# Kernel optimization log

Hardware: AMD Instinct MI355X
Metric: run time of the kernel (lower is better)

## Reference

```python
import jax, jax.numpy as jnp
import numpy as np

KEY_DIM = 512
VALUE_DIM = 128
CAPACITY = 500000
N_RETRIEVE = 16
LN_EPS = 1e-5
NORM_EPS = 1e-12


def _l2norm(x, axis=-1):
    # F.normalize: x / max(||x||, eps)
    n = jnp.sqrt(jnp.sum(x * x, axis=axis, keepdims=True))
    return x / jnp.maximum(n, NORM_EPS)


def setup_inputs() -> dict:
    key = jax.random.key(0)
    ks = jax.random.split(key, 5)
    s = 1.0 / np.sqrt(KEY_DIM)
    return {
        "query": jax.random.normal(ks[0], (1, KEY_DIM), jnp.float32),
        "W1": jax.random.normal(ks[1], (KEY_DIM, KEY_DIM), jnp.float32) * s,
        "b1": jnp.zeros((KEY_DIM,), jnp.float32),
        "W2": jax.random.normal(ks[2], (KEY_DIM, KEY_DIM), jnp.float32) * s,
        "b2": jnp.zeros((KEY_DIM,), jnp.float32),
        "gamma": jnp.ones((KEY_DIM,), jnp.float32),
        "beta": jnp.zeros((KEY_DIM,), jnp.float32),
        "keys": jax.random.normal(ks[3], (CAPACITY, KEY_DIM), jnp.float32),
        "values": jax.random.normal(ks[4], (CAPACITY, VALUE_DIM), jnp.float32),
    }


def reference(query, W1, b1, W2, b2, gamma, beta, keys, values):
    # read path detaches the query before projecting
    q = jax.lax.stop_gradient(query)                      # [1, D]
    h = jax.nn.silu(q @ W1.T + b1) @ W2.T + b2            # key_proj
    mu = jnp.mean(h, axis=-1, keepdims=True)
    var = jnp.var(h, axis=-1, keepdims=True)              # biased, like torch LN
    ln = (h - mu) / jnp.sqrt(var + LN_EPS) * gamma + beta
    qn = _l2norm(ln)[0]                                   # [D]
    kn = _l2norm(keys, axis=-1)                           # [N, D]
    sim = kn @ qn                                         # [N] cosine similarity
    top_sim, top_idx = jax.lax.top_k(sim, N_RETRIEVE)     # [k]
    attn = jax.nn.softmax(top_sim, axis=0)                # [k]
    vals = values[top_idx]                                # [k, V] gather
    out = attn @ vals                                     # [V] weighted sum
    return out
```

## Files before the change

kernel.cpp:

```cpp
#include <hip/hip_runtime.h>
#include <hip/hip_bf16.h>
#include <float.h>
#include <math.h>

#define KEY_DIM   512
#define VALUE_DIM 128
#define CAPACITY  500000
#define NRET      16

#define SUBROWS   8
#define NBLKS     512
#define NSUB      (CAPACITY / SUBROWS)
#define RING      4

#define AS3 __attribute__((address_space(3)))
#define AS1 __attribute__((address_space(1)))

__device__ __forceinline__ float wave_sum(float x) {
#pragma unroll
    for (int s = 32; s > 0; s >>= 1) x += __shfl_xor(x, s);
    return x;
}

template <bool SILU>
__global__ __launch_bounds__(256) void matvec512(
        const float* __restrict__ W, const float* __restrict__ x,
        const float* __restrict__ b, float* __restrict__ y) {
    const int wid  = threadIdx.x >> 6;
    const int lane = threadIdx.x & 63;
    const int r = blockIdx.x * 4 + wid;

    const float4* Wr = (const float4*)(W + (size_t)r * KEY_DIM);
    const float4* xv = (const float4*)x;

    float4 w0 = Wr[lane], w1 = Wr[lane + 64];
    float4 x0 = xv[lane], x1 = xv[lane + 64];

    float dot = w0.x * x0.x + w0.y * x0.y + w0.z * x0.z + w0.w * x0.w
              + w1.x * x1.x + w1.y * x1.y + w1.z * x1.z + w1.w * x1.w;
    dot = wave_sum(dot);

    if (lane == 0) {
        float v = dot + b[r];
        if (SILU) v = v / (1.0f + expf(-v));
        y[r] = v;
    }
}

__global__ __launch_bounds__(512) void ln_l2norm(
        const float* __restrict__ h, const float* __restrict__ gamma,
        const float* __restrict__ beta, float* __restrict__ qn) {
    __shared__ float s1[8], s2[8];
    const int t = threadIdx.x;
    const int wid = t >> 6, lane = t & 63;

    float x = h[t];
    float a = x, bb = x * x;
#pragma unroll
    for (int s = 32; s > 0; s >>= 1) { a += __shfl_xor(a, s); bb += __shfl_xor(bb, s); }
    if (lane == 0) { s1[wid] = a; s2[wid] = bb; }
    __syncthreads();

    float suma = 0.f, sumb = 0.f;
#pragma unroll
    for (int i = 0; i < 8; ++i) { suma += s1[i]; sumb += s2[i]; }
    float mu  = suma * (1.0f / KEY_DIM);
    float var = sumb * (1.0f / KEY_DIM) - mu * mu;
    float ln  = (x - mu) / sqrtf(var + 1e-5f) * gamma[t] + beta[t];

    float c = wave_sum(ln * ln);
    __syncthreads();
    if (lane == 0) s1[wid] = c;
    __syncthreads();
    float ss = 0.f;
#pragma unroll
    for (int i = 0; i < 8; ++i) ss += s1[i];
    float n = fmaxf(sqrtf(ss), 1e-12f);
    qn[t] = ln / n;
}

__global__ __launch_bounds__(256) void sim_topk(
        const float* __restrict__ keys, const float* __restrict__ qn,
        float* __restrict__ cand_v, int* __restrict__ cand_i) {
    __shared__ float kl[RING][SUBROWS][KEY_DIM];
    __shared__ float bv[64];
    __shared__ int   bi[64];

    const int tid  = threadIdx.x;
    const int w    = tid >> 6;
    const int lane = tid & 63;
    const int m    = lane & 31;
    const int rsel = lane >> 5;
    const int bid  = blockIdx.x;
    const int ns   = (NSUB - bid + NBLKS - 1) / NBLKS;
    const int s0   = (int)(((unsigned)bid * 7919u) % (unsigned)ns);

    float4 qr[4];
    {
        const float4* q4 = (const float4*)qn;
#pragma unroll
        for (int j = 0; j < 4; ++j) qr[j] = q4[4 * m + j];
    }

    int srcoff0, srcoff1;
    {
        int p0 = lane,      g0 = p0 >> 2, sl0 = p0 & 3;
        int p1 = 64 + lane, g1 = p1 >> 2, sl1 = p1 & 3;
        srcoff0 = (4 * g0 + ((sl0 - (g0 >> 1)) & 3)) * 16;
        srcoff1 = (4 * g1 + ((sl1 - (g1 >> 1)) & 3)) * 16;
    }
    int roff[4];
#pragma unroll
    for (int j = 0; j < 4; ++j) roff[j] = (4 * m + ((j + (m >> 1)) & 3)) * 16;

    float v[16]; int id[16];
#pragma unroll
    for (int j = 0; j < 16; ++j) { v[j] = -FLT_MAX; id[j] = 0x7fffffff; }

    auto stage = [&](int G, int slot) {
#pragma unroll
        for (int i = 0; i < 4; ++i) {
            const int rl = 2 * w + (i >> 1);
            const int h  = i & 1;
            const char* gp = (const char*)(keys + ((size_t)G * SUBROWS + rl) * KEY_DIM)
                             + (h ? srcoff1 : srcoff0);
            float* lp = &kl[slot][rl][h * 256];
            __builtin_amdgcn_global_load_lds((const AS1 float*)gp, (AS3 float*)lp,
                                             16, 0, 0);
        }
    };

    auto compute = [&](int G, int slot) {
        const char* rowbase = (const char*)&kl[slot][2 * w + rsel][0];
        float dot = 0.f, ss = 0.f;
#pragma unroll
        for (int j = 0; j < 4; ++j) {
            float4 k = *(const float4*)(rowbase + roff[j]);
            float4 q = qr[j];
            dot += k.x * q.x + k.y * q.y + k.z * q.z + k.w * q.w;
            ss  += k.x * k.x + k.y * k.y + k.z * k.z + k.w * k.w;
        }
#pragma unroll
        for (int s = 16; s > 0; s >>= 1) {
            dot += __shfl_xor(dot, s);
            ss  += __shfl_xor(ss, s);
        }
        float sim = dot / fmaxf(sqrtf(ss), 1e-12f);
#pragma unroll
        for (int q = 0; q < 2; ++q) {
            float sq = __shfl(sim, q * 32);
            if (sq > v[15]) {
                float cv = sq; int ci = G * SUBROWS + 2 * w + q;
#pragma unroll
                for (int jj = 0; jj < 16; ++jj) {
                    if (cv > v[jj]) {
                        float tv = v[jj]; int ti = id[jj];
                        v[jj] = cv; id[jj] = ci; cv = tv; ci = ti;
                    }
                }
            }
        }
    };

    {
        int se = s0;
        stage(bid + se * NBLKS, 0);
        se = (se + 1 >= ns) ? 0 : se + 1;
        stage(bid + se * NBLKS, 1);
        se = (se + 1 >= ns) ? 0 : se + 1;
        stage(bid + se * NBLKS, 2);
    }

    int scur = s0;
    int spre = s0 + 3; if (spre >= ns) spre -= ns;

#pragma unroll 1
    for (int s = 0; s < ns; ++s) {
        stage(bid + spre * NBLKS, (s + 3) & 3);
        spre = (spre + 1 >= ns) ? 0 : spre + 1;
        asm volatile("s_waitcnt vmcnt(12)" ::: "memory");
        __builtin_amdgcn_sched_barrier(0);
        compute(bid + scur * NBLKS, s & 3);
        __builtin_amdgcn_sched_barrier(0);
        scur = (scur + 1 >= ns) ? 0 : scur + 1;
    }

    asm volatile("s_waitcnt vmcnt(0)" ::: "memory");

    if (lane == 0) {
#pragma unroll
        for (int j = 0; j < 16; ++j) { bv[w * 16 + j] = v[j]; bi[w * 16 + j] = id[j]; }
    }
    __syncthreads();
    if (w == 0) {
        float lv = bv[lane]; int li = bi[lane];
        for (int rr = 0; rr < NRET; ++rr) {
            float mv = lv; int mi = li;
#pragma unroll
            for (int s = 32; s > 0; s >>= 1) {
                float ov = __shfl_xor(mv, s); int oi = __shfl_xor(mi, s);
                if (ov > mv || (ov == mv && oi < mi)) { mv = ov; mi = oi; }
            }
            if (lane == 0) {
                cand_v[bid * NRET + rr] = mv;
                cand_i[bid * NRET + rr] = mi;
            }
            if (lv == mv && li == mi) { lv = -FLT_MAX; li = 0x7fffffff; }
        }
    }
}

__global__ __launch_bounds__(256) void merge_out(
        const float* __restrict__ cand_v, const int* __restrict__ cand_i,
        const float* __restrict__ values, float* __restrict__ out) {
    const int tid  = threadIdx.x;
    const int wid  = tid >> 6;
    const int lane = tid & 63;
    const int M4 = (NBLKS * NRET) / 4;

    float v[16]; int id[16];
#pragma unroll
    for (int j = 0; j < 16; ++j) { v[j] = -FLT_MAX; id[j] = 0x7fffffff; }

    const float4* cv4 = (const float4*)cand_v;
    const int4*   ci4 = (const int4*)cand_i;
    for (int c = tid; c < M4; c += 256) {
        float4 cv = cv4[c]; int4 ci = ci4[c];
        float cvs[4] = {cv.x, cv.y, cv.z, cv.w};
        int   cis[4] = {ci.x, ci.y, ci.z, ci.w};
#pragma unroll
        for (int u = 0; u < 4; ++u) {
            float cu = cvs[u]; int iu = cis[u];
            if (cu > v[15]) {
#pragma unroll
                for (int j = 0; j < 16; ++j) {
                    if (cu > v[j]) {
                        float tv = v[j]; int ti = id[j];
                        v[j] = cu; id[j] = iu; cu = tv; iu = ti;
                    }
                }
            }
        }
    }

    __shared__ float sv[64];
    __shared__ int   si[64];
    for (int rr = 0; rr < NRET; ++rr) {
        float mv = v[0]; int mi = id[0];
#pragma unroll
        for (int s = 32; s > 0; s >>= 1) {
            float ov = __shfl_xor(mv, s); int oi = __shfl_xor(mi, s);
            if (ov > mv || (ov == mv && oi < mi)) { mv = ov; mi = oi; }
        }
        if (v[0] == mv && id[0] == mi) {
#pragma unroll
            for (int j = 0; j < 15; ++j) { v[j] = v[j + 1]; id[j] = id[j + 1]; }
            v[15] = -FLT_MAX; id[15] = 0x7fffffff;
        }
        if (lane == 0) { sv[wid * 16 + rr] = mv; si[wid * 16 + rr] = mi; }
    }
    __syncthreads();

    if (wid == 0) {
        float lv = sv[lane]; int li = si[lane];
        float sel_v = -FLT_MAX; int sel_i = 0;
        for (int rr = 0; rr < NRET; ++rr) {
            float mv = lv; int mi = li;
#pragma unroll
            for (int s = 32; s > 0; s >>= 1) {
                float ov = __shfl_xor(mv, s); int oi = __shfl_xor(mi, s);
                if (ov > mv || (ov == mv && oi < mi)) { mv = ov; mi = oi; }
            }
            if (lv == mv && li == mi) { lv = -FLT_MAX; li = 0x7fffffff; }
            if (lane == rr) { sel_v = mv; sel_i = mi; }
        }

        float m0 = __shfl(sel_v, 0);
        float e = (lane < NRET) ? expf(sel_v - m0) : 0.0f;
        float denom = wave_sum(e);

        float acc0 = 0.f, acc1 = 0.f;
        for (int rr = 0; rr < NRET; ++rr) {
            float ar = __shfl(e, rr) / denom;
            int   ir = __shfl(sel_i, rr);
            const float* vr = values + (size_t)ir * VALUE_DIM;
            acc0 += ar * vr[lane];
            acc1 += ar * vr[lane + 64];
        }
        out[lane]      = acc0;
        out[lane + 64] = acc1;
    }
}

extern "C" void kernel_launch(void* const* d_in, const int* in_sizes, int n_in,
                              void* d_out, int out_size, void* d_ws, size_t ws_size,
                              hipStream_t stream) {
    const float* query  = (const float*)d_in[0];
    const float* W1     = (const float*)d_in[1];
    const float* b1     = (const float*)d_in[2];
    const float* W2     = (const float*)d_in[3];
    const float* b2     = (const float*)d_in[4];
    const float* gamma  = (const float*)d_in[5];
    const float* beta   = (const float*)d_in[6];
    const float* keys   = (const float*)d_in[7];
    const float* values = (const float*)d_in[8];
    float* out = (float*)d_out;

    float* ws = (float*)d_ws;
    float* h1     = ws;
    float* h2     = ws + 512;
    float* qn     = ws + 1024;
    float* cand_v = ws + 2048;
    int*   cand_i = (int*)(ws + 2048 + NBLKS * NRET);

    matvec512<true ><<<128, 256, 0, stream>>>(W1, query, b1, h1);
    matvec512<false><<<128, 256, 0, stream>>>(W2, h1, b2, h2);
    ln_l2norm<<<1, 512, 0, stream>>>(h2, gamma, beta, qn);
    sim_topk<<<NBLKS, 256, 0, stream>>>(keys, qn, cand_v, cand_i);
    merge_out<<<1, 256, 0, stream>>>(cand_v, cand_i, values, out);
}
```

Baseline: 262.5 us.

## Split similarity scan between LDS-staged blocks and direct-load register blocks

The similarity/top-k kernel now launches 768 blocks. Two thirds of them stream a fixed 70 sub-tiles of 8 rows each through a 3-slot LDS ring using global_load_lds. The remaining third read the tail rows straight into registers, four rows per wave, and reduce with wave shuffles. The intent is to run two load paths side by side and raise the memory-level parallelism of a bandwidth-bound 1 GB scan. The cost is a hard-coded row split, a smaller prefetch ring, and more candidates for the single-block merge.

```diff
diff --git a/kernel.cpp b/kernel.cpp
--- a/kernel.cpp
+++ b/kernel.cpp
@@ -8,10 +8,15 @@
 #define CAPACITY  500000
 #define NRET      16
 
-#define SUBROWS   8
-#define NBLKS     512
-#define NSUB      (CAPACITY / SUBROWS)
-#define RING      4
+#define NBLKD     512
+#define NBLKV     256
+#define NBLKT     (NBLKD + NBLKV)
+#define NSD       70
+#define NDROWS    (NBLKD * NSD * 8)
+#define ROFF      NDROWS
+#define NVROWS    (CAPACITY - NDROWS)
+#define VSWEEP    (NBLKV * 4 * 4)
+#define RING      3
 
 #define AS3 __attribute__((address_space(3)))
 #define AS1 __attribute__((address_space(1)))
@@ -79,113 +84,156 @@
     qn[t] = ln / n;
 }
 
-__global__ __launch_bounds__(256) void sim_topk(
+__global__ __launch_bounds__(256) void sim_hybrid(
         const float* __restrict__ keys, const float* __restrict__ qn,
         float* __restrict__ cand_v, int* __restrict__ cand_i) {
-    __shared__ float kl[RING][SUBROWS][KEY_DIM];
+    __shared__ float kl[RING][8][KEY_DIM];
     __shared__ float bv[64];
     __shared__ int   bi[64];
 
     const int tid  = threadIdx.x;
     const int w    = tid >> 6;
     const int lane = tid & 63;
-    const int m    = lane & 31;
-    const int rsel = lane >> 5;
     const int bid  = blockIdx.x;
-    const int ns   = (NSUB - bid + NBLKS - 1) / NBLKS;
-    const int s0   = (int)(((unsigned)bid * 7919u) % (unsigned)ns);
-
-    float4 qr[4];
-    {
-        const float4* q4 = (const float4*)qn;
-#pragma unroll
-        for (int j = 0; j < 4; ++j) qr[j] = q4[4 * m + j];
-    }
-
-    int srcoff0, srcoff1;
-    {
-        int p0 = lane,      g0 = p0 >> 2, sl0 = p0 & 3;
-        int p1 = 64 + lane, g1 = p1 >> 2, sl1 = p1 & 3;
-        srcoff0 = (4 * g0 + ((sl0 - (g0 >> 1)) & 3)) * 16;
-        srcoff1 = (4 * g1 + ((sl1 - (g1 >> 1)) & 3)) * 16;
-    }
-    int roff[4];
-#pragma unroll
-    for (int j = 0; j < 4; ++j) roff[j] = (4 * m + ((j + (m >> 1)) & 3)) * 16;
+    const int r3   = bid % 3;
 
     float v[16]; int id[16];
 #pragma unroll
     for (int j = 0; j < 16; ++j) { v[j] = -FLT_MAX; id[j] = 0x7fffffff; }
 
-    auto stage = [&](int G, int slot) {
-#pragma unroll
-        for (int i = 0; i < 4; ++i) {
-            const int rl = 2 * w + (i >> 1);
-            const int h  = i & 1;
-            const char* gp = (const char*)(keys + ((size_t)G * SUBROWS + rl) * KEY_DIM)
-                             + (h ? srcoff1 : srcoff0);
-            float* lp = &kl[slot][rl][h * 256];
-            __builtin_amdgcn_global_load_lds((const AS1 float*)gp, (AS3 float*)lp,
-                                             16, 0, 0);
-        }
-    };
-
-    auto compute = [&](int G, int slot) {
-        const char* rowbase = (const char*)&kl[slot][2 * w + rsel][0];
-        float dot = 0.f, ss = 0.f;
-#pragma unroll
-        for (int j = 0; j < 4; ++j) {
-            float4 k = *(const float4*)(rowbase + roff[j]);
-            float4 q = qr[j];
-            dot += k.x * q.x + k.y * q.y + k.z * q.z + k.w * q.w;
-            ss  += k.x * k.x + k.y * k.y + k.z * k.z + k.w * k.w;
-        }
-#pragma unroll
-        for (int s = 16; s > 0; s >>= 1) {
-            dot += __shfl_xor(dot, s);
-            ss  += __shfl_xor(ss, s);
-        }
-        float sim = dot / fmaxf(sqrtf(ss), 1e-12f);
-#pragma unroll
-        for (int q = 0; q < 2; ++q) {
-            float sq = __shfl(sim, q * 32);
-            if (sq > v[15]) {
-                float cv = sq; int ci = G * SUBROWS + 2 * w + q;
-#pragma unroll
-                for (int jj = 0; jj < 16; ++jj) {
-                    if (cv > v[jj]) {
-                        float tv = v[jj]; int ti = id[jj];
-                        v[jj] = cv; id[jj] = ci; cv = tv; ci = ti;
+    if (r3 < 2) {
+        const int d    = (bid / 3) * 2 + r3;
+        const int m    = lane & 31;
+        const int rsel = lane >> 5;
+        const int s0   = (d * 7919) % NSD;
+
+        float4 qr[4];
+        {
+            const float4* q4 = (const float4*)qn;
+#pragma unroll
+            for (int j = 0; j < 4; ++j) qr[j] = q4[4 * m + j];
+        }
+        int srcoff0, srcoff1;
+        {
+            int p0 = lane,      g0 = p0 >> 2, sl0 = p0 & 3;
+            int p1 = 64 + lane, g1 = p1 >> 2, sl1 = p1 & 3;
+            srcoff0 = (4 * g0 + ((sl0 - (g0 >> 1)) & 3)) * 16;
+            srcoff1 = (4 * g1 + ((sl1 - (g1 >> 1)) & 3)) * 16;
+        }
+        int roff[4];
+#pragma unroll
+        for (int j = 0; j < 4; ++j) roff[j] = (4 * m + ((j + (m >> 1)) & 3)) * 16;
+
+        auto stage = [&](int G, int slot) {
+#pragma unroll
+            for (int i = 0; i < 4; ++i) {
+                const int rl = 2 * w + (i >> 1);
+                const int h  = i & 1;
+                const char* gp = (const char*)(keys + ((size_t)G * 8 + rl) * KEY_DIM)
+                                 + (h ? srcoff1 : srcoff0);
+                float* lp = &kl[slot][rl][h * 256];
+                __builtin_amdgcn_global_load_lds((const AS1 float*)gp, (AS3 float*)lp,
+                                                 16, 0, 0);
+            }
+        };
+        auto compute = [&](int G, int slot) {
+            const char* rowbase = (const char*)&kl[slot][2 * w + rsel][0];
+            float dot = 0.f, ss = 0.f;
+#pragma unroll
+            for (int j = 0; j < 4; ++j) {
+                float4 k = *(const float4*)(rowbase + roff[j]);
+                float4 q = qr[j];
+                dot += k.x * q.x + k.y * q.y + k.z * q.z + k.w * q.w;
+                ss  += k.x * k.x + k.y * k.y + k.z * k.z + k.w * k.w;
+            }
+#pragma unroll
+            for (int s = 16; s > 0; s >>= 1) {
+                dot += __shfl_xor(dot, s);
+                ss  += __shfl_xor(ss, s);
+            }
+            float sim = dot / fmaxf(sqrtf(ss), 1e-12f);
+#pragma unroll
+            for (int q = 0; q < 2; ++q) {
+                float sq = __shfl(sim, q * 32);
+                if (sq > v[15]) {
+                    float cv = sq; int ci = G * 8 + 2 * w + q;
+#pragma unroll
+                    for (int jj = 0; jj < 16; ++jj) {
+                        if (cv > v[jj]) {
+                            float tv = v[jj]; int ti = id[jj];
+                            v[jj] = cv; id[jj] = ci; cv = tv; ci = ti;
+                        }
                     }
                 }
             }
-        }
-    };
-
-    {
-        int se = s0;
-        stage(bid + se * NBLKS, 0);
-        se = (se + 1 >= ns) ? 0 : se + 1;
-        stage(bid + se * NBLKS, 1);
-        se = (se + 1 >= ns) ? 0 : se + 1;
-        stage(bid + se * NBLKS, 2);
-    }
-
-    int scur = s0;
-    int spre = s0 + 3; if (spre >= ns) spre -= ns;
+        };
+
+        {
+            int se = s0;
+            stage(d + se * NBLKD, 0);
+            se = (se + 1 >= NSD) ? 0 : se + 1;
+            stage(d + se * NBLKD, 1);
+        }
+        int scur = s0;
+        int spre = s0 + 2; if (spre >= NSD) spre -= NSD;
 
 #pragma unroll 1
-    for (int s = 0; s < ns; ++s) {
-        stage(bid + spre * NBLKS, (s + 3) & 3);
-        spre = (spre + 1 >= ns) ? 0 : spre + 1;
-        asm volatile("s_waitcnt vmcnt(12)" ::: "memory");
-        __builtin_amdgcn_sched_barrier(0);
-        compute(bid + scur * NBLKS, s & 3);
-        __builtin_amdgcn_sched_barrier(0);
-        scur = (scur + 1 >= ns) ? 0 : scur + 1;
-    }
-
-    asm volatile("s_waitcnt vmcnt(0)" ::: "memory");
+        for (int s = 0; s < NSD; ++s) {
+            stage(d + spre * NBLKD, (s + 2) % 3);
+            spre = (spre + 1 >= NSD) ? 0 : spre + 1;
+            asm volatile("s_waitcnt vmcnt(8)" ::: "memory");
+            __builtin_amdgcn_sched_barrier(0);
+            compute(d + scur * NBLKD, s % 3);
+            __builtin_amdgcn_sched_barrier(0);
+            scur = (scur + 1 >= NSD) ? 0 : scur + 1;
+        }
+        asm volatile("s_waitcnt vmcnt(0)" ::: "memory");
+    } else {
+        const int gw = (bid / 3) * 4 + w;
+        const float4* q4 = (const float4*)qn;
+        float4 q0 = q4[lane], q1 = q4[lane + 64];
+
+#pragma unroll 1
+        for (int base = gw * 4; base < NVROWS; base += VSWEEP) {
+            float4 ka[4], kb[4];
+#pragma unroll
+            for (int j = 0; j < 4; ++j) {
+                const float4* kp = (const float4*)(keys + (size_t)(ROFF + base + j) * KEY_DIM);
+                ka[j] = kp[lane];
+                kb[j] = kp[lane + 64];
+            }
+            float dot[4], ss[4];
+#pragma unroll
+            for (int j = 0; j < 4; ++j) {
+                dot[j] = ka[j].x * q0.x + ka[j].y * q0.y + ka[j].z * q0.z + ka[j].w * q0.w
+                       + kb[j].x * q1.x + kb[j].y * q1.y + kb[j].z * q1.z + kb[j].w * q1.w;
+                ss[j]  = ka[j].x * ka[j].x + ka[j].y * ka[j].y + ka[j].z * ka[j].z + ka[j].w * ka[j].w
+                       + kb[j].x * kb[j].x + kb[j].y * kb[j].y + kb[j].z * kb[j].z + kb[j].w * kb[j].w;
+            }
+#pragma unroll
+            for (int s = 32; s > 0; s >>= 1) {
+#pragma unroll
+                for (int j = 0; j < 4; ++j) {
+                    dot[j] += __shfl_xor(dot[j], s);
+                    ss[j]  += __shfl_xor(ss[j], s);
+                }
+            }
+#pragma unroll
+            for (int j = 0; j < 4; ++j) {
+                float sim = dot[j] / fmaxf(sqrtf(ss[j]), 1e-12f);
+                if (sim > v[15]) {
+                    float cv = sim; int ci = ROFF + base + j;
+#pragma unroll
+                    for (int jj = 0; jj < 16; ++jj) {
+                        if (cv > v[jj]) {
+                            float tv = v[jj]; int ti = id[jj];
+                            v[jj] = cv; id[jj] = ci; cv = tv; ci = ti;
+                        }
+                    }
+                }
+            }
+        }
+    }
 
     if (lane == 0) {
 #pragma unroll
@@ -193,6 +241,7 @@
     }
     __syncthreads();
     if (w == 0) {
+        const int cidx = (r3 < 2) ? ((bid / 3) * 2 + r3) : (NBLKD + bid / 3);
         float lv = bv[lane]; int li = bi[lane];
         for (int rr = 0; rr < NRET; ++rr) {
             float mv = lv; int mi = li;
@@ -202,8 +251,8 @@
                 if (ov > mv || (ov == mv && oi < mi)) { mv = ov; mi = oi; }
             }
             if (lane == 0) {
-                cand_v[bid * NRET + rr] = mv;
-                cand_i[bid * NRET + rr] = mi;
+                cand_v[cidx * NRET + rr] = mv;
+                cand_i[cidx * NRET + rr] = mi;
             }
             if (lv == mv && li == mi) { lv = -FLT_MAX; li = 0x7fffffff; }
         }
@@ -216,7 +265,7 @@
     const int tid  = threadIdx.x;
     const int wid  = tid >> 6;
     const int lane = tid & 63;
-    const int M4 = (NBLKS * NRET) / 4;
+    const int M4 = (NBLKT * NRET) / 4;
 
     float v[16]; int id[16];
 #pragma unroll
@@ -311,11 +360,11 @@
     float* h2     = ws + 512;
     float* qn     = ws + 1024;
     float* cand_v = ws + 2048;
-    int*   cand_i = (int*)(ws + 2048 + NBLKS * NRET);
+    int*   cand_i = (int*)(ws + 2048 + NBLKT * NRET);
 
     matvec512<true ><<<128, 256, 0, stream>>>(W1, query, b1, h1);
     matvec512<false><<<128, 256, 0, stream>>>(W2, h1, b2, h2);
     ln_l2norm<<<1, 512, 0, stream>>>(h2, gamma, beta, qn);
-    sim_topk<<<NBLKS, 256, 0, stream>>>(keys, qn, cand_v, cand_i);
+    sim_hybrid<<<NBLKT, 256, 0, stream>>>(keys, qn, cand_v, cand_i);
     merge_out<<<1, 256, 0, stream>>>(cand_v, cand_i, values, out);
 }
```

Measured after the change: 313.1 us. 19.3% more time.
